# Performance work log

Measured on AMD Instinct MI355X. Metric: run time of the kernel, lower is better.

## Reference

```python
import jax, jax.numpy as jnp
import numpy as np

B, S, H = 1, 2048, 1024          # batch, seq_len, hidden_dim
E, I = 16, 512                    # num_experts, moe_intermediate_size
TOP_K = 4
NORM_TOPK_PROB = True


def setup_inputs() -> dict:
    key = jax.random.key(0)
    k0, k1, k2, k3, k4 = jax.random.split(key, 5)
    scale = 0.02
    return {
        "hidden_states": jax.random.normal(k0, (B, S, H), jnp.float32),
        "w_gate": jax.random.normal(k1, (H, E), jnp.float32) * scale,
        "w_gate_proj": jax.random.normal(k2, (E, H, I), jnp.float32) * scale,
        "w_up_proj": jax.random.normal(k3, (E, H, I), jnp.float32) * scale,
        "w_down_proj": jax.random.normal(k4, (E, I, H), jnp.float32) * scale,
    }


def reference(hidden_states, w_gate, w_gate_proj, w_up_proj, w_down_proj):
    b, s, h = hidden_states.shape
    x = hidden_states.reshape(-1, h)                      # [T, H]
    T = x.shape[0]

    router_logits = x @ w_gate                            # [T, E]
    routing_weights = jax.nn.softmax(router_logits.astype(jnp.float32), axis=-1)
    top_w, sel = jax.lax.top_k(routing_weights, TOP_K)    # [T, K]
    if NORM_TOPK_PROB:
        top_w = top_w / top_w.sum(axis=-1, keepdims=True)
    top_w = top_w.astype(x.dtype)

    # Per-token combine weight for every expert (0 if not in top-k).
    # Mathematically identical to the sort/gather/index_add dispatch loop.
    combine = jnp.zeros((T, E), x.dtype).at[
        jnp.arange(T)[:, None], sel].set(top_w)           # [T, E]

    def expert_step(acc, inp):
        wg, wu, wd, w = inp                               # [H,I],[H,I],[I,H],[T]
        hidden = jax.nn.silu(x @ wg) * (x @ wu)           # [T, I]
        return acc + (hidden @ wd) * w[:, None], None

    out0 = jnp.zeros_like(x)
    out, _ = jax.lax.scan(
        expert_step, out0,
        (w_gate_proj, w_up_proj, w_down_proj, combine.T))
    return out.reshape(b, s, h), router_logits
```

## Files before the change

kernel.cpp:

```cpp
#include <hip/hip_runtime.h>
#include <math.h>

constexpr int TT = 2048;
constexpr int HH = 1024;
constexpr int EE = 16;
constexpr int II = 512;

typedef unsigned short u16;
typedef short s16x8 __attribute__((ext_vector_type(8)));
typedef float f32x4 __attribute__((ext_vector_type(4)));

__device__ __forceinline__ u16 f2bf(float f) {
  unsigned u = __float_as_uint(f);
  u = (u + 0x7fffu + ((u >> 16) & 1u)) >> 16;
  return (u16)u;
}

__device__ __forceinline__ void gl2lds16(const void* g, void* l) {
  __builtin_amdgcn_global_load_lds(
      (const __attribute__((address_space(1))) unsigned*)g,
      (__attribute__((address_space(3))) unsigned*)l, 16, 0, 0);
}

__global__ void cast_x_kernel(const float* __restrict__ x, u16* __restrict__ xb,
                              const float* __restrict__ wg, float* __restrict__ wgT) {
  int b = blockIdx.x;
  if (b < TT * HH / 1024) {
    int i = b * blockDim.x + threadIdx.x;
    float4 v = reinterpret_cast<const float4*>(x)[i];
    ushort4 o;
    o.x = f2bf(v.x); o.y = f2bf(v.y); o.z = f2bf(v.z); o.w = f2bf(v.w);
    reinterpret_cast<ushort4*>(xb)[i] = o;
  } else {
    int i = (b - TT * HH / 1024) * blockDim.x + threadIdx.x;
    int h = i >> 4, e = i & 15;
    wgT[e * HH + h] = wg[i];
  }
}

__global__ __launch_bounds__(256) void wtrans_kernel(
    const float* __restrict__ wgp, const float* __restrict__ wup,
    const float* __restrict__ wdp, u16* __restrict__ wgt,
    u16* __restrict__ wut, u16* __restrict__ wdt) {
  int z = blockIdx.z;
  int e = z & 15, t = z >> 4;
  const float* src; u16* dst; int K, N;
  if (t == 0)      { src = wgp + (size_t)e * HH * II; dst = wgt + (size_t)e * II * HH; K = HH; N = II; }
  else if (t == 1) { src = wup + (size_t)e * HH * II; dst = wut + (size_t)e * II * HH; K = HH; N = II; }
  else             { src = wdp + (size_t)e * II * HH; dst = wdt + (size_t)e * HH * II; K = II; N = HH; }
  int bx = blockIdx.x, by = blockIdx.y;
  if (bx * 64 >= N || by * 64 >= K) return;
  int K0 = by * 64, N0 = bx * 64;

  __shared__ u16 lds[64 * 64];

  int tid = threadIdx.x;
  int KR  = tid >> 4;
  int nc4 = (tid & 15) * 4;
  float4 r[4];
#pragma unroll
  for (int ii = 0; ii < 4; ++ii)
    r[ii] = *reinterpret_cast<const float4*>(&src[(size_t)(K0 + 4 * KR + ii) * N + N0 + nc4]);
  u16 bv[4][4];
#pragma unroll
  for (int ii = 0; ii < 4; ++ii) {
    bv[ii][0] = f2bf(r[ii].x); bv[ii][1] = f2bf(r[ii].y);
    bv[ii][2] = f2bf(r[ii].z); bv[ii][3] = f2bf(r[ii].w);
  }
#pragma unroll
  for (int j = 0; j < 4; ++j) {
    int n = nc4 + j;
    int a = n * 64 + ((KR ^ (n & 15)) << 2);
    uint2 p;
    p.x = (unsigned)bv[0][j] | ((unsigned)bv[1][j] << 16);
    p.y = (unsigned)bv[2][j] | ((unsigned)bv[3][j] << 16);
    *reinterpret_cast<uint2*>(&lds[a]) = p;
  }
  __syncthreads();
  int n  = tid >> 2;
  int kc = tid & 3;
  int m  = n & 15;
#pragma unroll
  for (int c = 0; c < 2; ++c) {
    int g = 4 * c + kc;
    int a0 = n * 64 + (((2 * g)     ^ m) << 2);
    int a1 = n * 64 + (((2 * g + 1) ^ m) << 2);
    uint2 q0 = *reinterpret_cast<const uint2*>(&lds[a0]);
    uint2 q1 = *reinterpret_cast<const uint2*>(&lds[a1]);
    uint4 st; st.x = q0.x; st.y = q0.y; st.z = q1.x; st.w = q1.y;
    *reinterpret_cast<uint4*>(&dst[(size_t)(N0 + n) * K + K0 + 8 * g]) = st;
  }
}

__global__ void router_kernel(const float* __restrict__ x, const float* __restrict__ wgT,
                              float* __restrict__ rl, unsigned* __restrict__ selmask,
                              float* __restrict__ wsel) {
  int lane = threadIdx.x & 63, wv = threadIdx.x >> 6;
  int t = blockIdx.x * 4 + wv;
  const float* xr = x + (size_t)t * HH;
  float xv[16];
#pragma unroll
  for (int i = 0; i < 16; ++i) xv[i] = xr[lane + 64 * i];
  float lg[16];
#pragma unroll
  for (int e = 0; e < 16; ++e) {
    const float* wr = wgT + (size_t)e * HH;
    float p = 0.f;
#pragma unroll
    for (int i = 0; i < 16; ++i) p += xv[i] * wr[lane + 64 * i];
#pragma unroll
    for (int s = 32; s > 0; s >>= 1) p += __shfl_xor(p, s, 64);
    lg[e] = p;
  }
  if (lane < 16) rl[(size_t)t * 16 + lane] = lg[lane];
  unsigned mask = 0;
  int sel[4]; float bl[4];
#pragma unroll
  for (int k = 0; k < 4; ++k) {
    float best = -3.4e38f; int bi = 0;
#pragma unroll
    for (int e = 0; e < 16; ++e) {
      bool ok = !((mask >> e) & 1u) && (lg[e] > best);
      best = ok ? lg[e] : best;
      bi = ok ? e : bi;
    }
    mask |= 1u << bi;
    sel[k] = bi; bl[k] = best;
  }
  float mx = bl[0];
  float wk[4]; float s = 0.f;
#pragma unroll
  for (int k = 0; k < 4; ++k) { wk[k] = expf(bl[k] - mx); s += wk[k]; }
  float inv = 1.f / s;
  if (lane == 0) {
    selmask[t] = (unsigned)sel[0] | ((unsigned)sel[1] << 4) |
                 ((unsigned)sel[2] << 8) | ((unsigned)sel[3] << 12);
    float4 w4 = make_float4(wk[0] * inv, wk[1] * inv, wk[2] * inv, wk[3] * inv);
    reinterpret_cast<float4*>(wsel)[t] = w4;
  }
}

__global__ void build_lists_kernel(const unsigned* __restrict__ selmask,
                                   const float* __restrict__ wsel,
                                   int* __restrict__ counts, int* __restrict__ offsets,
                                   int* __restrict__ tlist, float* __restrict__ wlist) {
  __shared__ int scnt[16];
  int lane = threadIdx.x & 63, e = threadIdx.x >> 6;
  int base = 0;
  for (int t0 = 0; t0 < TT; t0 += 64) {
    int t = t0 + lane;
    unsigned m = selmask[t];
    int k = -1;
#pragma unroll
    for (int j = 0; j < 4; ++j)
      if (((m >> (4 * j)) & 15u) == (unsigned)e) k = j;
    unsigned long long bal = __ballot(k >= 0);
    int pos = base + (int)__popcll(bal & ((1ull << lane) - 1ull));
    if (k >= 0) {
      tlist[e * TT + pos] = t;
      wlist[e * TT + pos] = wsel[t * 4 + k];
    }
    base += (int)__popcll(bal);
  }
  if (lane == 0) scnt[e] = base;
  __syncthreads();
  if (threadIdx.x == 0) {
    int s = 0;
    for (int i = 0; i < 16; ++i) { counts[i] = scnt[i]; offsets[i] = s; s += scnt[i]; }
    offsets[16] = s;
  }
}

__global__ __launch_bounds__(256, 2) void gateup_kernel(
    const u16* __restrict__ xb, const u16* __restrict__ wgt, const u16* __restrict__ wut,
    const int* __restrict__ counts, const int* __restrict__ offsets,
    const int* __restrict__ tlist, const float* __restrict__ wlist,
    u16* __restrict__ hidden) {
  int e = blockIdx.z, mt = blockIdx.y, nt = blockIdx.x;
  int cnt = counts[e];
  if (mt * 128 >= cnt) return;
  __shared__ u16 As[128 * 64];
  __shared__ u16 Bg[128 * 64];
  __shared__ u16 Bu[128 * 64];
  int tid = threadIdx.x, lane = tid & 63, wv = tid >> 6;
  int wm = wv >> 1, wn = wv & 1;
  int srow = lane >> 3;
  int scol = (lane & 7) * 8;
  const u16* wgE = wgt + (size_t)e * II * HH;
  const u16* wuE = wut + (size_t)e * II * HH;
  const u16* gA[4]; const u16* gBg[4]; const u16* gBu[4];
#pragma unroll
  for (int c = 0; c < 4; ++c) {
    int chunk = c * 4 + wv;
    int m = chunk * 8 + srow;
    int mi = mt * 128 + m; if (mi >= cnt) mi = cnt - 1;
    int tok = tlist[e * TT + mi];
    gA[c]  = xb  + (size_t)tok * HH + scol;
    int n = nt * 128 + chunk * 8 + srow;
    gBg[c] = wgE + (size_t)n * HH + scol;
    gBu[c] = wuE + (size_t)n * HH + scol;
  }
  f32x4 accG[4][4] = {}; f32x4 accU[4][4] = {};
  for (int k0 = 0; k0 < HH; k0 += 64) {
#pragma unroll
    for (int c = 0; c < 4; ++c) {
      int chunk = c * 4 + wv;
      gl2lds16(gA[c]  + k0, &As[chunk * 512]);
      gl2lds16(gBg[c] + k0, &Bg[chunk * 512]);
      gl2lds16(gBu[c] + k0, &Bu[chunk * 512]);
    }
    __syncthreads();
#pragma unroll
    for (int kk = 0; kk < 64; kk += 32) {
      s16x8 a[4], bg[4], bu[4];
      int koff = kk + (lane >> 4) * 8;
#pragma unroll
      for (int f = 0; f < 4; ++f) {
        a[f]  = *reinterpret_cast<const s16x8*>(&As[(wm * 64 + f * 16 + (lane & 15)) * 64 + koff]);
        bg[f] = *reinterpret_cast<const s16x8*>(&Bg[(wn * 64 + f * 16 + (lane & 15)) * 64 + koff]);
        bu[f] = *reinterpret_cast<const s16x8*>(&Bu[(wn * 64 + f * 16 + (lane & 15)) * 64 + koff]);
      }
#pragma unroll
      for (int fm = 0; fm < 4; ++fm)
#pragma unroll
        for (int fn = 0; fn < 4; ++fn) {
          accG[fm][fn] = __builtin_amdgcn_mfma_f32_16x16x32_bf16(a[fm], bg[fn], accG[fm][fn], 0, 0, 0);
          accU[fm][fn] = __builtin_amdgcn_mfma_f32_16x16x32_bf16(a[fm], bu[fn], accU[fm][fn], 0, 0, 0);
        }
    }
    __syncthreads();
  }
  int hb = offsets[e];
  int quad = lane >> 4, colc = lane & 15;
#pragma unroll
  for (int fm = 0; fm < 4; ++fm) {
#pragma unroll
    for (int r = 0; r < 4; ++r) {
      int mi = mt * 128 + wm * 64 + fm * 16 + quad * 4 + r;
      if (mi < cnt) {
        float wr = wlist[e * TT + mi];
        u16* hrow = hidden + (size_t)(hb + mi) * II + nt * 128 + wn * 64;
#pragma unroll
        for (int fn = 0; fn < 4; ++fn) {
          float g = accG[fm][fn][r], u = accU[fm][fn][r];
          float hval = wr * u * g / (1.f + expf(-g));
          hrow[fn * 16 + colc] = f2bf(hval);
        }
      }
    }
  }
}

__global__ __launch_bounds__(256, 2) void down_kernel(
    const u16* __restrict__ hidden, const u16* __restrict__ wdt,
    const int* __restrict__ counts, const int* __restrict__ offsets,
    const int* __restrict__ tlist, float* __restrict__ out) {
  int e = blockIdx.z, mt = blockIdx.y, nt = blockIdx.x;
  int cnt = counts[e];
  if (mt * 128 >= cnt) return;
  int hb = offsets[e];
  __shared__ u16 As[128 * 64];
  __shared__ u16 Bs[128 * 64];
  int tid = threadIdx.x, lane = tid & 63, wv = tid >> 6;
  int wm = wv >> 1, wn = wv & 1;
  int srow = lane >> 3, scol = (lane & 7) * 8;
  const u16* wdE = wdt + (size_t)e * HH * II;
  const u16* gA[4]; const u16* gB[4];
#pragma unroll
  for (int c = 0; c < 4; ++c) {
    int chunk = c * 4 + wv;
    int row = hb + mt * 128 + chunk * 8 + srow;
    if (row > 8191) row = 8191;
    gA[c] = hidden + (size_t)row * II + scol;
    int n = nt * 128 + chunk * 8 + srow;
    gB[c] = wdE + (size_t)n * II + scol;
  }
  f32x4 acc[4][4] = {};
  for (int k0 = 0; k0 < II; k0 += 64) {
#pragma unroll
    for (int c = 0; c < 4; ++c) {
      int chunk = c * 4 + wv;
      gl2lds16(gA[c] + k0, &As[chunk * 512]);
      gl2lds16(gB[c] + k0, &Bs[chunk * 512]);
    }
    __syncthreads();
#pragma unroll
    for (int kk = 0; kk < 64; kk += 32) {
      s16x8 a[4], b[4];
      int koff = kk + (lane >> 4) * 8;
#pragma unroll
      for (int f = 0; f < 4; ++f) {
        a[f] = *reinterpret_cast<const s16x8*>(&As[(wm * 64 + f * 16 + (lane & 15)) * 64 + koff]);
        b[f] = *reinterpret_cast<const s16x8*>(&Bs[(wn * 64 + f * 16 + (lane & 15)) * 64 + koff]);
      }
#pragma unroll
      for (int fm = 0; fm < 4; ++fm)
#pragma unroll
        for (int fn = 0; fn < 4; ++fn)
          acc[fm][fn] = __builtin_amdgcn_mfma_f32_16x16x32_bf16(a[fm], b[fn], acc[fm][fn], 0, 0, 0);
    }
    __syncthreads();
  }
  int quad = lane >> 4, colc = lane & 15;
#pragma unroll
  for (int fm = 0; fm < 4; ++fm) {
#pragma unroll
    for (int r = 0; r < 4; ++r) {
      int mi = mt * 128 + wm * 64 + fm * 16 + quad * 4 + r;
      if (mi < cnt) {
        int tok = tlist[e * TT + mi];
        float* orow = out + (size_t)tok * HH + nt * 128 + wn * 64;
#pragma unroll
        for (int fn = 0; fn < 4; ++fn)
          atomicAdd(&orow[fn * 16 + colc], acc[fm][fn][r]);
      }
    }
  }
}

extern "C" void kernel_launch(void* const* d_in, const int* in_sizes, int n_in,
                              void* d_out, int out_size, void* d_ws, size_t ws_size,
                              hipStream_t stream) {
  const float* x   = (const float*)d_in[0];
  const float* wg  = (const float*)d_in[1];
  const float* wgp = (const float*)d_in[2];
  const float* wup = (const float*)d_in[3];
  const float* wdp = (const float*)d_in[4];
  float* out = (float*)d_out;
  float* rl  = out + (size_t)TT * HH;

  char* w = (char*)d_ws;
  int*      counts  = (int*)(w + 0);
  int*      offsets = (int*)(w + 64);
  unsigned* selmask = (unsigned*)(w + 1024);
  float*    wsel    = (float*)(w + 1024 + 8192);
  int*      tlist   = (int*)(w + 49152);
  float*    wlist   = (float*)(w + 49152 + 131072);
  float*    wgT     = (float*)(w + 49152 + 262144);
  u16*      xb      = (u16*)(w + 49152 + 262144 + 65536);
  u16*      wgt     = xb  + (size_t)TT * HH;
  u16*      wut     = wgt + (size_t)EE * II * HH;
  u16*      wdt     = wut + (size_t)EE * II * HH;
  u16*      hidden  = wdt + (size_t)EE * HH * II;

  hipMemsetAsync(out, 0, (size_t)TT * HH * sizeof(float), stream);

  hipLaunchKernelGGL(cast_x_kernel, dim3(TT * HH / 1024 + 64), dim3(256), 0, stream,
                     x, xb, wg, wgT);
  hipLaunchKernelGGL(wtrans_kernel, dim3(16, 16, 48), dim3(256), 0, stream,
                     wgp, wup, wdp, wgt, wut, wdt);
  hipLaunchKernelGGL(router_kernel, dim3(TT / 4), dim3(256), 0, stream,
                     x, wgT, rl, selmask, wsel);
  hipLaunchKernelGGL(build_lists_kernel, dim3(1), dim3(1024), 0, stream,
                     selmask, wsel, counts, offsets, tlist, wlist);
  hipLaunchKernelGGL(gateup_kernel, dim3(4, 16, 16), dim3(256), 0, stream,
                     xb, wgt, wut, counts, offsets, tlist, wlist, hidden);
  hipLaunchKernelGGL(down_kernel, dim3(8, 16, 16), dim3(256), 0, stream,
                     hidden, wdt, counts, offsets, tlist, out);
}
```

Before: 262.6 us.

## XOR-swizzle LDS tiles and halve gate/up N-tile to 64

Applies an XOR swizzle to the 16-byte column groups when loading global data into LDS, and to the matching reads in both the gate/up and down GEMM kernels. This is meant to remove LDS bank conflicts on the MFMA fragment reads. The gate/up kernel also shrinks its N tile from 128 to 64 and doubles the grid in x. That cuts LDS use and accumulator registers, which should help occupancy and spread work across more blocks. In exchange, each token row of x is reloaded twice as often.

```diff
diff --git a/kernel.cpp b/kernel.cpp
--- a/kernel.cpp
+++ b/kernel.cpp
@@ -21,6 +21,7 @@
       (const __attribute__((address_space(1))) unsigned*)g,
       (__attribute__((address_space(3))) unsigned*)l, 16, 0, 0);
 }
+
 
 __global__ void cast_x_kernel(const float* __restrict__ x, u16* __restrict__ xb,
                               const float* __restrict__ wg, float* __restrict__ wgT) {
@@ -180,50 +181,63 @@
   int cnt = counts[e];
   if (mt * 128 >= cnt) return;
   __shared__ u16 As[128 * 64];
-  __shared__ u16 Bg[128 * 64];
-  __shared__ u16 Bu[128 * 64];
+  __shared__ u16 Bg[64 * 64];
+  __shared__ u16 Bu[64 * 64];
   int tid = threadIdx.x, lane = tid & 63, wv = tid >> 6;
   int wm = wv >> 1, wn = wv & 1;
   int srow = lane >> 3;
-  int scol = (lane & 7) * 8;
+  int scol = (((lane & 7) ^ srow)) * 8;
   const u16* wgE = wgt + (size_t)e * II * HH;
   const u16* wuE = wut + (size_t)e * II * HH;
-  const u16* gA[4]; const u16* gBg[4]; const u16* gBu[4];
-#pragma unroll
-  for (int c = 0; c < 4; ++c) {
+  const u16* gp[8];
+#pragma unroll
+  for (int c = 0; c < 8; ++c) {
     int chunk = c * 4 + wv;
-    int m = chunk * 8 + srow;
-    int mi = mt * 128 + m; if (mi >= cnt) mi = cnt - 1;
-    int tok = tlist[e * TT + mi];
-    gA[c]  = xb  + (size_t)tok * HH + scol;
-    int n = nt * 128 + chunk * 8 + srow;
-    gBg[c] = wgE + (size_t)n * HH + scol;
-    gBu[c] = wuE + (size_t)n * HH + scol;
-  }
-  f32x4 accG[4][4] = {}; f32x4 accU[4][4] = {};
+    const u16* p;
+    if (chunk < 16) {
+      int mi = mt * 128 + chunk * 8 + srow; if (mi >= cnt) mi = cnt - 1;
+      int tok = tlist[e * TT + mi];
+      p = xb + (size_t)tok * HH + scol;
+    } else if (chunk < 24) {
+      int n = nt * 64 + (chunk - 16) * 8 + srow;
+      p = wgE + (size_t)n * HH + scol;
+    } else {
+      int n = nt * 64 + (chunk - 24) * 8 + srow;
+      p = wuE + (size_t)n * HH + scol;
+    }
+    gp[c] = p;
+  }
+  f32x4 accG[4][2] = {}; f32x4 accU[4][2] = {};
+  int quad = lane >> 4, colc = lane & 15;
   for (int k0 = 0; k0 < HH; k0 += 64) {
 #pragma unroll
-    for (int c = 0; c < 4; ++c) {
+    for (int c = 0; c < 8; ++c) {
       int chunk = c * 4 + wv;
-      gl2lds16(gA[c]  + k0, &As[chunk * 512]);
-      gl2lds16(gBg[c] + k0, &Bg[chunk * 512]);
-      gl2lds16(gBu[c] + k0, &Bu[chunk * 512]);
+      u16* dst = (chunk < 16) ? &As[chunk * 512]
+               : (chunk < 24) ? &Bg[(chunk - 16) * 512]
+                              : &Bu[(chunk - 24) * 512];
+      gl2lds16(gp[c] + k0, dst);
     }
     __syncthreads();
 #pragma unroll
     for (int kk = 0; kk < 64; kk += 32) {
-      s16x8 a[4], bg[4], bu[4];
-      int koff = kk + (lane >> 4) * 8;
+      int gl = (kk >> 3) + quad;
+      s16x8 a[4], bg[2], bu[2];
 #pragma unroll
       for (int f = 0; f < 4; ++f) {
-        a[f]  = *reinterpret_cast<const s16x8*>(&As[(wm * 64 + f * 16 + (lane & 15)) * 64 + koff]);
-        bg[f] = *reinterpret_cast<const s16x8*>(&Bg[(wn * 64 + f * 16 + (lane & 15)) * 64 + koff]);
-        bu[f] = *reinterpret_cast<const s16x8*>(&Bu[(wn * 64 + f * 16 + (lane & 15)) * 64 + koff]);
+        int m = wm * 64 + f * 16 + colc;
+        a[f] = *reinterpret_cast<const s16x8*>(&As[m * 64 + ((gl ^ (m & 7)) << 3)]);
+      }
+#pragma unroll
+      for (int f = 0; f < 2; ++f) {
+        int n = wn * 32 + f * 16 + colc;
+        bg[f] = *reinterpret_cast<const s16x8*>(&Bg[n * 64 + ((gl ^ (n & 7)) << 3)]);
+        bu[f] = *reinterpret_cast<const s16x8*>(&Bu[n * 64 + ((gl ^ (n & 7)) << 3)]);
       }
 #pragma unroll
       for (int fm = 0; fm < 4; ++fm)
 #pragma unroll
-        for (int fn = 0; fn < 4; ++fn) {
+        for (int fn = 0; fn < 2; ++fn) {
           accG[fm][fn] = __builtin_amdgcn_mfma_f32_16x16x32_bf16(a[fm], bg[fn], accG[fm][fn], 0, 0, 0);
           accU[fm][fn] = __builtin_amdgcn_mfma_f32_16x16x32_bf16(a[fm], bu[fn], accU[fm][fn], 0, 0, 0);
         }
@@ -231,7 +245,6 @@
     __syncthreads();
   }
   int hb = offsets[e];
-  int quad = lane >> 4, colc = lane & 15;
 #pragma unroll
   for (int fm = 0; fm < 4; ++fm) {
 #pragma unroll
@@ -239,9 +252,9 @@
       int mi = mt * 128 + wm * 64 + fm * 16 + quad * 4 + r;
       if (mi < cnt) {
         float wr = wlist[e * TT + mi];
-        u16* hrow = hidden + (size_t)(hb + mi) * II + nt * 128 + wn * 64;
-#pragma unroll
-        for (int fn = 0; fn < 4; ++fn) {
+        u16* hrow = hidden + (size_t)(hb + mi) * II + nt * 64 + wn * 32;
+#pragma unroll
+        for (int fn = 0; fn < 2; ++fn) {
           float g = accG[fm][fn][r], u = accU[fm][fn][r];
           float hval = wr * u * g / (1.f + expf(-g));
           hrow[fn * 16 + colc] = f2bf(hval);
@@ -263,7 +276,8 @@
   __shared__ u16 Bs[128 * 64];
   int tid = threadIdx.x, lane = tid & 63, wv = tid >> 6;
   int wm = wv >> 1, wn = wv & 1;
-  int srow = lane >> 3, scol = (lane & 7) * 8;
+  int srow = lane >> 3;
+  int scol = (((lane & 7) ^ srow)) * 8;
   const u16* wdE = wdt + (size_t)e * HH * II;
   const u16* gA[4]; const u16* gB[4];
 #pragma unroll
@@ -276,6 +290,7 @@
     gB[c] = wdE + (size_t)n * II + scol;
   }
   f32x4 acc[4][4] = {};
+  int quad = lane >> 4, colc = lane & 15;
   for (int k0 = 0; k0 < II; k0 += 64) {
 #pragma unroll
     for (int c = 0; c < 4; ++c) {
@@ -286,12 +301,14 @@
     __syncthreads();
 #pragma unroll
     for (int kk = 0; kk < 64; kk += 32) {
+      int gl = (kk >> 3) + quad;
       s16x8 a[4], b[4];
-      int koff = kk + (lane >> 4) * 8;
 #pragma unroll
       for (int f = 0; f < 4; ++f) {
-        a[f] = *reinterpret_cast<const s16x8*>(&As[(wm * 64 + f * 16 + (lane & 15)) * 64 + koff]);
-        b[f] = *reinterpret_cast<const s16x8*>(&Bs[(wn * 64 + f * 16 + (lane & 15)) * 64 + koff]);
+        int m = wm * 64 + f * 16 + colc;
+        int n = wn * 64 + f * 16 + colc;
+        a[f] = *reinterpret_cast<const s16x8*>(&As[m * 64 + ((gl ^ (m & 7)) << 3)]);
+        b[f] = *reinterpret_cast<const s16x8*>(&Bs[n * 64 + ((gl ^ (n & 7)) << 3)]);
       }
 #pragma unroll
       for (int fm = 0; fm < 4; ++fm)
@@ -301,7 +318,6 @@
     }
     __syncthreads();
   }
-  int quad = lane >> 4, colc = lane & 15;
 #pragma unroll
   for (int fm = 0; fm < 4; ++fm) {
 #pragma unroll
@@ -353,7 +369,7 @@
                      x, wgT, rl, selmask, wsel);
   hipLaunchKernelGGL(build_lists_kernel, dim3(1), dim3(1024), 0, stream,
                      selmask, wsel, counts, offsets, tlist, wlist);
-  hipLaunchKernelGGL(gateup_kernel, dim3(4, 16, 16), dim3(256), 0, stream,
+  hipLaunchKernelGGL(gateup_kernel, dim3(8, 16, 16), dim3(256), 0, stream,
                      xb, wgt, wut, counts, offsets, tlist, wlist, hidden);
   hipLaunchKernelGGL(down_kernel, dim3(8, 16, 16), dim3(256), 0, stream,
                      hidden, wdt, counts, offsets, tlist, out);
```

Measured after the change: 255.8 us. 1.03x faster.
